# Optimization experiments

Hardware: AMD Instinct MI355X
Metric: run time of the kernel (lower is better)

The kernel has to match this reference:

```python
import jax, jax.numpy as jnp
import numpy as np

N_NODES = 100_000
N_EDGES = 1_600_000
D = 128
BN_EPS = 1e-5
GIN_EPS = 0.0  # GINConv default eps, train_eps=False


def setup_inputs() -> dict:
    key = jax.random.key(0)
    ks = jax.random.split(key, 8)
    x = jax.random.normal(ks[0], (N_NODES, D), dtype=jnp.float32)
    edge_index = jax.random.randint(ks[1], (2, N_EDGES), 0, N_NODES, dtype=jnp.int64)
    s = 1.0 / np.sqrt(D)
    W1 = jax.random.uniform(ks[2], (D, D), jnp.float32, -s, s)
    b1 = jax.random.uniform(ks[3], (D,), jnp.float32, -s, s)
    W2 = jax.random.uniform(ks[4], (D, D), jnp.float32, -s, s)
    b2 = jax.random.uniform(ks[5], (D,), jnp.float32, -s, s)
    W3 = jax.random.uniform(ks[6], (D, D), jnp.float32, -s, s)
    g1 = jnp.ones((D,), jnp.float32)
    be1 = jnp.zeros((D,), jnp.float32)
    g2 = jnp.ones((D,), jnp.float32)
    be2 = jnp.zeros((D,), jnp.float32)
    return {"x": x, "edge_index": edge_index,
            "W1": W1, "b1": b1, "g1": g1, "be1": be1,
            "W2": W2, "b2": b2, "g2": g2, "be2": be2,
            "W3": W3}


def _batchnorm(h, gamma, beta):
    # training-mode BatchNorm1d over node dim with biased variance
    mean = jnp.mean(h, axis=0)
    var = jnp.mean(jnp.square(h - mean), axis=0)
    return (h - mean) * jax.lax.rsqrt(var + BN_EPS) * gamma + beta


def reference(x, edge_index, W1, b1, g1, be1, W2, b2, g2, be2, W3):
    src, dst = edge_index[0], edge_index[1]
    # GIN aggregation: (1+eps)*x_i + sum_{j->i} x_j  (scatter-add over edges)
    agg = jax.ops.segment_sum(x[src], dst, num_segments=N_NODES)
    h = (1.0 + GIN_EPS) * x + agg
    # MLP: Linear+BN+ReLU x2, then Linear (no bias)
    h = jax.nn.relu(_batchnorm(h @ W1.T + b1, g1, be1))
    h = jax.nn.relu(_batchnorm(h @ W2.T + b2, g2, be2))
    h = h @ W3.T
    # GINLayer final activation (bn=None)
    return jax.nn.relu(h)
```

## Files before the change

### kernel.cpp

```cpp
#include <hip/hip_runtime.h>

#define NN 100000
#define NE 1600000
#define DD 128
#define NCB 196
#define TILE 2048
#define NTILE 782
#define SREP 32
#define WPAD 17408

typedef __attribute__((ext_vector_type(8))) short bf16x8;
typedef __attribute__((ext_vector_type(4))) float f32x4;

union u4bf8 { uint4 u; bf16x8 v; };

__device__ __forceinline__ ushort f2bf(float f) {
    union { float f; uint i; } v; v.f = f;
    uint i = v.i;
    return (ushort)((i + 0x7fffu + ((i >> 16) & 1u)) >> 16);
}
__device__ __forceinline__ float bf2f(ushort u) {
    union { uint i; float f; } v; v.i = ((uint)u) << 16; return v.f;
}
__device__ __forceinline__ float blo(uint v) { return bf2f((ushort)(v & 0xffffu)); }
__device__ __forceinline__ float bhi(uint v) { return bf2f((ushort)(v >> 16)); }

__global__ __launch_bounds__(256) void k_xbh(const float* __restrict__ x,
                                             uint* __restrict__ xb,
                                             const int* __restrict__ ei,
                                             int* __restrict__ ghistP,
                                             const float* __restrict__ W1,
                                             const float* __restrict__ W2,
                                             const float* __restrict__ W3,
                                             ushort* __restrict__ Wbp) {
    __shared__ int h[NCB];
    int t = threadIdx.x;
    if (t < NCB) h[t] = 0;
    __syncthreads();
    int base = blockIdx.x * TILE;
#pragma unroll
    for (int i = 0; i < 8; ++i) {
        int e = base + i * 256 + t;
        if (e < NE) atomicAdd(&h[ei[NE + e] >> 9], 1);
    }
    int gid = blockIdx.x * 256 + t;
#pragma unroll
    for (int i = 0; i < 8; ++i) {
        int item = i * (NTILE * 256) + gid;
        if (item < NN * 16) {
            int n = item >> 4, q = item & 15;
            const float* xp = x + (size_t)n * DD + q * 8;
            float4 a = *(const float4*)xp;
            float4 b = *(const float4*)(xp + 4);
            uint4 pk;
            pk.x = (uint)f2bf(a.x) | ((uint)f2bf(a.y) << 16);
            pk.y = (uint)f2bf(a.z) | ((uint)f2bf(a.w) << 16);
            pk.z = (uint)f2bf(b.x) | ((uint)f2bf(b.y) << 16);
            pk.w = (uint)f2bf(b.z) | ((uint)f2bf(b.w) << 16);
            *(uint4*)(xb + (size_t)n * 64 + q * 4) = pk;
        }
    }
    int c = gid;
    if (c < 6144) {
        int l = c >> 11;
        int cc = c & 2047;
        int r = cc >> 4, c8 = (cc & 15) * 8;
        const float* Wl = (l == 0) ? W1 : (l == 1) ? W2 : W3;
        const float* p = Wl + r * DD + c8;
        float4 a = *(const float4*)p;
        float4 b = *(const float4*)(p + 4);
        uint4 pk;
        pk.x = (uint)f2bf(a.x) | ((uint)f2bf(a.y) << 16);
        pk.y = (uint)f2bf(a.z) | ((uint)f2bf(a.w) << 16);
        pk.z = (uint)f2bf(b.x) | ((uint)f2bf(b.y) << 16);
        pk.w = (uint)f2bf(b.z) | ((uint)f2bf(b.w) << 16);
        *(uint4*)&Wbp[(size_t)l * WPAD + r * 136 + c8] = pk;
    }
    __syncthreads();
    if (t < NCB && h[t] > 0) atomicAdd(&ghistP[t * 16], h[t]);
}

__global__ void k_cscan(const int* __restrict__ ghistP, int* __restrict__ cb,
                        int* __restrict__ gcurP) {
    __shared__ int sh[256];
    int t = threadIdx.x;
    int my = (t < NCB) ? ghistP[t * 16] : 0;
    sh[t] = my;
    __syncthreads();
    for (int o = 1; o < 256; o <<= 1) {
        int u = (t >= o) ? sh[t - o] : 0;
        __syncthreads();
        sh[t] += u;
        __syncthreads();
    }
    if (t < NCB) { int ex = sh[t] - my; cb[t] = ex; gcurP[t * 16] = ex; }
    if (t == NCB - 1) cb[NCB] = sh[t];
}

__global__ __launch_bounds__(256) void k_cscatter(const int* __restrict__ ei,
                                                  int* __restrict__ gcurP,
                                                  uint* __restrict__ buck) {
    __shared__ int h[NCB];
    __shared__ int tb[NCB];
    int t = threadIdx.x;
    if (t < NCB) h[t] = 0;
    __syncthreads();
    int base = blockIdx.x * TILE;
    uint vv[8]; int bb[8], rr[8];
#pragma unroll
    for (int i = 0; i < 8; ++i) {
        int e = base + i * 256 + t;
        bb[i] = -1;
        if (e < NE) {
            int s = ei[e], d = ei[NE + e];
            int b = d >> 9;
            bb[i] = b;
            vv[i] = (uint)s | ((uint)(d & 511) << 17);
            rr[i] = atomicAdd(&h[b], 1);
        }
    }
    __syncthreads();
    if (t < NCB && h[t] > 0) tb[t] = atomicAdd(&gcurP[t * 16], h[t]);
    __syncthreads();
#pragma unroll
    for (int i = 0; i < 8; ++i) {
        if (bb[i] >= 0) buck[tb[bb[i]] + rr[i]] = vv[i];
    }
}

__global__ __launch_bounds__(256) void k_fsort(const uint* __restrict__ buck,
                                               const int* __restrict__ cb,
                                               int* __restrict__ csr,
                                               int* __restrict__ rowp) {
    __shared__ int cnt[512];
    __shared__ int sd[256];
    int c = blockIdx.x, t = threadIdx.x;
    cnt[t] = 0; cnt[t + 256] = 0;
    __syncthreads();
    int s0 = cb[c], s1 = cb[c + 1];
    for (int i = s0 + t; i < s1; i += 256)
        atomicAdd(&cnt[(buck[i] >> 17) & 511], 1);
    __syncthreads();
    int p = cnt[2 * t], q = cnt[2 * t + 1];
    sd[t] = p + q;
    __syncthreads();
    for (int o = 1; o < 256; o <<= 1) {
        int u = (t >= o) ? sd[t - o] : 0;
        __syncthreads();
        sd[t] += u;
        __syncthreads();
    }
    int base = sd[t] - (p + q);
    rowp[c * 512 + 2 * t]     = s0 + base;
    rowp[c * 512 + 2 * t + 1] = s0 + base + p;
    __syncthreads();
    cnt[2 * t] = base;
    cnt[2 * t + 1] = base + p;
    __syncthreads();
    for (int i = s0 + t; i < s1; i += 256) {
        uint v = buck[i];
        int ld = (int)((v >> 17) & 511u);
        int pos = atomicAdd(&cnt[ld], 1);
        csr[s0 + pos] = (int)(v & 0x1FFFFu);
    }
}

#define B8(ACC0, ACC1, SJ, J)                                               \
    {                                                                       \
        int s0 = __shfl(SJ, J),     s1 = __shfl(SJ, J + 1);                 \
        int s2 = __shfl(SJ, J + 2), s3 = __shfl(SJ, J + 3);                 \
        int s4 = __shfl(SJ, J + 4), s5 = __shfl(SJ, J + 5);                 \
        int s6 = __shfl(SJ, J + 6), s7 = __shfl(SJ, J + 7);                 \
        uint v0 = xb[(size_t)s0 * 64 + lane], v1 = xb[(size_t)s1 * 64 + lane]; \
        uint v2 = xb[(size_t)s2 * 64 + lane], v3 = xb[(size_t)s3 * 64 + lane]; \
        uint v4 = xb[(size_t)s4 * 64 + lane], v5 = xb[(size_t)s5 * 64 + lane]; \
        uint v6 = xb[(size_t)s6 * 64 + lane], v7 = xb[(size_t)s7 * 64 + lane]; \
        ACC0 += blo(v0) + blo(v1) + blo(v2) + blo(v3)                       \
              + blo(v4) + blo(v5) + blo(v6) + blo(v7);                      \
        ACC1 += bhi(v0) + bhi(v1) + bhi(v2) + bhi(v3)                       \
              + bhi(v4) + bhi(v5) + bhi(v6) + bhi(v7);                      \
    }

__global__ __launch_bounds__(256) void k_gather(const uint* __restrict__ xb,
                                                const int* __restrict__ rowp,
                                                const int* __restrict__ csr,
                                                ushort* __restrict__ agg) {
    const int HALF = NN / 2;
    int wave = threadIdx.x >> 6, lane = threadIdx.x & 63;
    int w = blockIdx.x * 4 + wave;
    if (w >= HALF) return;
    int nA = w, nB = w + HALF;
    uint sA = xb[(size_t)nA * 64 + lane];
    uint sB = xb[(size_t)nB * 64 + lane];
    float a0 = blo(sA), a1 = bhi(sA);
    float b0 = blo(sB), b1 = bhi(sB);
    int iA = rowp[nA], eA = rowp[nA + 1];
    int iB = rowp[nB], eB = rowp[nB + 1];

    while (iA < eA || iB < eB) {
        int mA = eA - iA; if (mA > 64) mA = 64; if (mA < 0) mA = 0;
        int mB = eB - iB; if (mB > 64) mB = 64; if (mB < 0) mB = 0;
        int sjA = (lane < mA) ? csr[iA + lane] : 0;
        int sjB = (lane < mB) ? csr[iB + lane] : 0;
        int j = 0, k = 0;
        while (j + 8 <= mA && k + 8 <= mB) {
            int t0 = __shfl(sjA, j),     t1 = __shfl(sjA, j + 1);
            int t2 = __shfl(sjA, j + 2), t3 = __shfl(sjA, j + 3);
            int t4 = __shfl(sjA, j + 4), t5 = __shfl(sjA, j + 5);
            int t6 = __shfl(sjA, j + 6), t7 = __shfl(sjA, j + 7);
            int u0 = __shfl(sjB, k),     u1 = __shfl(sjB, k + 1);
            int u2 = __shfl(sjB, k + 2), u3 = __shfl(sjB, k + 3);
            int u4 = __shfl(sjB, k + 4), u5 = __shfl(sjB, k + 5);
            int u6 = __shfl(sjB, k + 6), u7 = __shfl(sjB, k + 7);
            uint vA0 = xb[(size_t)t0 * 64 + lane], vA1 = xb[(size_t)t1 * 64 + lane];
            uint vA2 = xb[(size_t)t2 * 64 + lane], vA3 = xb[(size_t)t3 * 64 + lane];
            uint vA4 = xb[(size_t)t4 * 64 + lane], vA5 = xb[(size_t)t5 * 64 + lane];
            uint vA6 = xb[(size_t)t6 * 64 + lane], vA7 = xb[(size_t)t7 * 64 + lane];
            uint vB0 = xb[(size_t)u0 * 64 + lane], vB1 = xb[(size_t)u1 * 64 + lane];
            uint vB2 = xb[(size_t)u2 * 64 + lane], vB3 = xb[(size_t)u3 * 64 + lane];
            uint vB4 = xb[(size_t)u4 * 64 + lane], vB5 = xb[(size_t)u5 * 64 + lane];
            uint vB6 = xb[(size_t)u6 * 64 + lane], vB7 = xb[(size_t)u7 * 64 + lane];
            a0 += blo(vA0) + blo(vA1) + blo(vA2) + blo(vA3)
                + blo(vA4) + blo(vA5) + blo(vA6) + blo(vA7);
            a1 += bhi(vA0) + bhi(vA1) + bhi(vA2) + bhi(vA3)
                + bhi(vA4) + bhi(vA5) + bhi(vA6) + bhi(vA7);
            b0 += blo(vB0) + blo(vB1) + blo(vB2) + blo(vB3)
                + blo(vB4) + blo(vB5) + blo(vB6) + blo(vB7);
            b1 += bhi(vB0) + bhi(vB1) + bhi(vB2) + bhi(vB3)
                + bhi(vB4) + bhi(vB5) + bhi(vB6) + bhi(vB7);
            j += 8; k += 8;
        }
        while (j + 8 <= mA) { B8(a0, a1, sjA, j) j += 8; }
        while (k + 8 <= mB) { B8(b0, b1, sjB, k) k += 8; }
        while (j < mA && k < mB) {
            int t = __shfl(sjA, j); int u = __shfl(sjB, k);
            uint vA = xb[(size_t)t * 64 + lane];
            uint vB = xb[(size_t)u * 64 + lane];
            a0 += blo(vA); a1 += bhi(vA);
            b0 += blo(vB); b1 += bhi(vB);
            ++j; ++k;
        }
        while (j < mA) {
            int t = __shfl(sjA, j++);
            uint vA = xb[(size_t)t * 64 + lane];
            a0 += blo(vA); a1 += bhi(vA);
        }
        while (k < mB) {
            int u = __shfl(sjB, k++);
            uint vB = xb[(size_t)u * 64 + lane];
            b0 += blo(vB); b1 += bhi(vB);
        }
        iA += mA; iB += mB;
    }

    uint pkA = (uint)f2bf(a0) | ((uint)f2bf(a1) << 16);
    uint pkB = (uint)f2bf(b0) | ((uint)f2bf(b1) << 16);
    ((uint*)(agg + (size_t)nA * DD))[lane] = pkA;
    ((uint*)(agg + (size_t)nB * DD))[lane] = pkB;
}

template <int MODE>
__global__ __launch_bounds__(256) void k_gemm(const ushort* __restrict__ Ain,
                                              const ushort* __restrict__ Wp,
                                              const float* __restrict__ bias,
                                              const float* __restrict__ statsIn,
                                              const float* __restrict__ g,
                                              const float* __restrict__ be,
                                              void* __restrict__ Outv,
                                              float* __restrict__ statsOut) {
    __shared__ __align__(16) char smem[DD * 136 * 2];
    ushort* lw = (ushort*)smem;
    float* sm32 = (float*)smem;
    __shared__ float red[2][4][DD];
    __shared__ float lac[2 * DD];

    int tid = threadIdx.x;
#pragma unroll
    for (int it = 0; it < 8; ++it) {
        int o8 = (it * 256 + tid) * 8;
        *(uint4*)&lw[o8] = *(const uint4*)&Wp[o8];
    }
    if (tid < 128) {
        int o8 = 16384 + tid * 8;
        *(uint4*)&lw[o8] = *(const uint4*)&Wp[o8];
    }
    if constexpr (MODE != 1) {
        if (tid < DD) {
            float S = 0.f, Q = 0.f;
#pragma unroll
            for (int r = 0; r < SREP; ++r) {
                S += statsIn[(r << 8) + tid];
                Q += statsIn[(r << 8) + DD + tid];
            }
            float inv = 1.f / (float)NN;
            float mean = S * inv;
            float var = Q * inv - mean * mean;
            float a = g[tid] * rsqrtf(var + 1e-5f);
            lac[tid] = a;
            lac[DD + tid] = be[tid] - mean * a;
        }
    }
    __syncthreads();

    int wave = tid >> 6, lane = tid & 63;
    int lm = lane & 15, quad = lane >> 4;
    int row0 = blockIdx.x * 64 + wave * 16;
    int arow = row0 + lm;
    int ar = (arow < NN) ? arow : 0;

    bf16x8 afrag[4];
#pragma unroll
    for (int kb = 0; kb < 4; ++kb) {
        int k0 = kb * 32 + quad * 8;
        const ushort* ap = Ain + (size_t)ar * DD + k0;
        u4bf8 u; u.u = *(const uint4*)ap;
        if constexpr (MODE == 1) {
            afrag[kb] = u.v;
        } else {
            uint pk[4] = {u.u.x, u.u.y, u.u.z, u.u.w};
            bf16x8 af;
#pragma unroll
            for (int jj = 0; jj < 4; ++jj) {
                int k = k0 + jj * 2;
                float v0 = blo(pk[jj]);
                float v1 = bhi(pk[jj]);
                v0 = fmaxf(fmaf(v0, lac[k], lac[DD + k]), 0.f);
                v1 = fmaxf(fmaf(v1, lac[k + 1], lac[DD + k + 1]), 0.f);
                af[jj * 2]     = (short)f2bf(v0);
                af[jj * 2 + 1] = (short)f2bf(v1);
            }
            afrag[kb] = af;
        }
    }

    f32x4 acc[8];
#pragma unroll
    for (int nt = 0; nt < 8; ++nt) {
        float bv = (MODE == 3) ? 0.f : bias[nt * 16 + lm];
        acc[nt] = (f32x4){bv, bv, bv, bv};
    }

#pragma unroll
    for (int kb = 0; kb < 4; ++kb) {
#pragma unroll
        for (int nt = 0; nt < 8; ++nt) {
            bf16x8 bfrag = *(const bf16x8*)&lw[(nt * 16 + lm) * 136 + kb * 32 + quad * 8];
            acc[nt] = __builtin_amdgcn_mfma_f32_16x16x32_bf16(afrag[kb], bfrag, acc[nt], 0, 0, 0);
        }
    }

    float csum[8], csq[8];
    if constexpr (MODE != 3) {
#pragma unroll
        for (int nt = 0; nt < 8; ++nt) {
            float s = 0.f, q = 0.f;
#pragma unroll
            for (int r = 0; r < 4; ++r) {
                int row = row0 + quad * 4 + r;
                float v = acc[nt][r];
                if (row < NN) { s += v; q += v * v; }
            }
            csum[nt] = s; csq[nt] = q;
        }
    }

    __syncthreads();
#pragma unroll
    for (int nt = 0; nt < 8; ++nt) {
#pragma unroll
        for (int r = 0; r < 4; ++r) {
            int lrow = wave * 16 + quad * 4 + r;
            float v = acc[nt][r];
            if (MODE == 3) v = fmaxf(v, 0.f);
            sm32[lrow * 132 + nt * 16 + lm] = v;
        }
    }
    __syncthreads();

    {
        int row = tid >> 2, seg = tid & 3;
        int grow = blockIdx.x * 64 + row;
        if (grow < NN) {
            const float* rp = sm32 + row * 132 + seg * 32;
            if constexpr (MODE == 3) {
                float* Out32 = (float*)Outv;
#pragma unroll
                for (int u = 0; u < 8; ++u) {
                    float4 o;
                    o.x = rp[u * 4]; o.y = rp[u * 4 + 1];
                    o.z = rp[u * 4 + 2]; o.w = rp[u * 4 + 3];
                    *(float4*)&Out32[(size_t)grow * DD + seg * 32 + u * 4] = o;
                }
            } else {
                ushort* Out16 = (ushort*)Outv;
#pragma unroll
                for (int u = 0; u < 4; ++u) {
                    uint4 pk;
                    pk.x = (uint)f2bf(rp[u * 8])     | ((uint)f2bf(rp[u * 8 + 1]) << 16);
                    pk.y = (uint)f2bf(rp[u * 8 + 2]) | ((uint)f2bf(rp[u * 8 + 3]) << 16);
                    pk.z = (uint)f2bf(rp[u * 8 + 4]) | ((uint)f2bf(rp[u * 8 + 5]) << 16);
                    pk.w = (uint)f2bf(rp[u * 8 + 6]) | ((uint)f2bf(rp[u * 8 + 7]) << 16);
                    *(uint4*)&Out16[(size_t)grow * DD + seg * 32 + u * 8] = pk;
                }
            }
        }
    }

    if constexpr (MODE != 3) {
#pragma unroll
        for (int nt = 0; nt < 8; ++nt) {
            float s = csum[nt], q = csq[nt];
            s += __shfl_down(s, 16, 64); q += __shfl_down(q, 16, 64);
            s += __shfl_down(s, 32, 64); q += __shfl_down(q, 32, 64);
            if (quad == 0) {
                red[0][wave][nt * 16 + lm] = s;
                red[1][wave][nt * 16 + lm] = q;
            }
        }
        __syncthreads();
        if (tid < DD) {
            float S = red[0][0][tid] + red[0][1][tid] + red[0][2][tid] + red[0][3][tid];
            float Q = red[1][0][tid] + red[1][1][tid] + red[1][2][tid] + red[1][3][tid];
            int rep = (blockIdx.x & (SREP - 1)) << 8;
            atomicAdd(&statsOut[rep + tid], S);
            atomicAdd(&statsOut[rep + DD + tid], Q);
        }
    }
}

extern "C" void kernel_launch(void* const* d_in, const int* in_sizes, int n_in,
                              void* d_out, int out_size, void* d_ws, size_t ws_size,
                              hipStream_t stream) {
    const float* x   = (const float*)d_in[0];
    const int* ei    = (const int*)d_in[1];
    const float* W1  = (const float*)d_in[2];
    const float* b1  = (const float*)d_in[3];
    const float* g1  = (const float*)d_in[4];
    const float* be1 = (const float*)d_in[5];
    const float* W2  = (const float*)d_in[6];
    const float* b2  = (const float*)d_in[7];
    const float* g2  = (const float*)d_in[8];
    const float* be2 = (const float*)d_in[9];
    const float* W3  = (const float*)d_in[10];

    float* stats  = (float*)d_ws;
    float* stats2 = stats + SREP * 256;
    int* ghistP   = (int*)(stats2 + SREP * 256);
    ushort* Wbp   = (ushort*)(ghistP + NCB * 16);
    int* cb       = (int*)(Wbp + 3 * WPAD);
    int* gcurP    = cb + NCB + 4;
    int* rowp     = gcurP + NCB * 16;
    uint* buck    = (uint*)(rowp + NCB * 512 + 4);
    int* csr      = (int*)(buck + NE);
    ushort* agg   = (ushort*)(((uintptr_t)(csr + NE) + 15) & ~(uintptr_t)15);
    uint* xb     = (uint*)d_out;
    ushort* t1   = (ushort*)d_out + (size_t)NN * DD;
    ushort* t2   = agg;
    float* outp  = (float*)d_out;

    int gblk = (NN + 63) / 64;
    hipMemsetAsync(stats, 0, (2 * SREP * 256) * sizeof(float) + NCB * 16 * sizeof(int), stream);
    k_xbh<<<NTILE, 256, 0, stream>>>(x, xb, ei, ghistP, W1, W2, W3, Wbp);
    k_cscan<<<1, 256, 0, stream>>>(ghistP, cb, gcurP);
    k_cscatter<<<NTILE, 256, 0, stream>>>(ei, gcurP, buck);
    k_fsort<<<NCB, 256, 0, stream>>>(buck, cb, csr, rowp);
    k_gather<<<(NN / 2 + 3) / 4, 256, 0, stream>>>(xb, rowp, csr, agg);
    k_gemm<1><<<gblk, 256, 0, stream>>>(agg, Wbp, b1, nullptr, nullptr, nullptr, t1, stats);
    k_gemm<2><<<gblk, 256, 0, stream>>>(t1, Wbp + WPAD, b2, stats, g1, be1, t2, stats2);
    k_gemm<3><<<gblk, 256, 0, stream>>>(t2, Wbp + 2 * WPAD, nullptr, stats2, g2, be2, outp, nullptr);
}
```

Measured before the change: 313.7 us.

## Process four row sub-tiles per GEMM block and store results directly

Each GEMM block now handles 256 rows in four 64-row sub-tiles, so the 128x128 weight tile is loaded into LDS once per 256 rows instead of once per 64 rows, and there are a quarter as many blocks. The LDS staging of the output tile and its coalesced vector stores are removed; each lane writes scalar bf16 or fp32 values straight to global memory. This cuts weight reloads and block-level syncs, but the direct stores are narrow and strided (2-byte writes across 16 columns), which may coalesce poorly. Fewer blocks also reduces parallelism.

```diff
diff --git a/kernel.cpp b/kernel.cpp
--- a/kernel.cpp
+++ b/kernel.cpp
@@ -8,6 +8,7 @@
 #define NTILE 782
 #define SREP 32
 #define WPAD 17408
+#define GROWS 256
 
 typedef __attribute__((ext_vector_type(8))) short bf16x8;
 typedef __attribute__((ext_vector_type(4))) float f32x4;
@@ -268,9 +269,7 @@
                                               const float* __restrict__ be,
                                               void* __restrict__ Outv,
                                               float* __restrict__ statsOut) {
-    __shared__ __align__(16) char smem[DD * 136 * 2];
-    ushort* lw = (ushort*)smem;
-    float* sm32 = (float*)smem;
+    __shared__ __align__(16) ushort lw[DD * 136];
     __shared__ float red[2][4][DD];
     __shared__ float lac[2 * DD];
 
@@ -304,103 +303,73 @@
 
     int wave = tid >> 6, lane = tid & 63;
     int lm = lane & 15, quad = lane >> 4;
-    int row0 = blockIdx.x * 64 + wave * 16;
-    int arow = row0 + lm;
-    int ar = (arow < NN) ? arow : 0;
-
-    bf16x8 afrag[4];
-#pragma unroll
-    for (int kb = 0; kb < 4; ++kb) {
-        int k0 = kb * 32 + quad * 8;
-        const ushort* ap = Ain + (size_t)ar * DD + k0;
-        u4bf8 u; u.u = *(const uint4*)ap;
-        if constexpr (MODE == 1) {
-            afrag[kb] = u.v;
-        } else {
-            uint pk[4] = {u.u.x, u.u.y, u.u.z, u.u.w};
-            bf16x8 af;
-#pragma unroll
-            for (int jj = 0; jj < 4; ++jj) {
-                int k = k0 + jj * 2;
-                float v0 = blo(pk[jj]);
-                float v1 = bhi(pk[jj]);
-                v0 = fmaxf(fmaf(v0, lac[k], lac[DD + k]), 0.f);
-                v1 = fmaxf(fmaf(v1, lac[k + 1], lac[DD + k + 1]), 0.f);
-                af[jj * 2]     = (short)f2bf(v0);
-                af[jj * 2 + 1] = (short)f2bf(v1);
+    ushort* Out16 = (ushort*)Outv;
+    float* Out32 = (float*)Outv;
+
+    float csum[8], csq[8];
+#pragma unroll
+    for (int nt = 0; nt < 8; ++nt) { csum[nt] = 0.f; csq[nt] = 0.f; }
+
+#pragma unroll
+    for (int sub = 0; sub < 4; ++sub) {
+        int row0 = blockIdx.x * GROWS + sub * 64 + wave * 16;
+        int arow = row0 + lm;
+        int ar = (arow < NN) ? arow : 0;
+
+        bf16x8 afrag[4];
+#pragma unroll
+        for (int kb = 0; kb < 4; ++kb) {
+            int k0 = kb * 32 + quad * 8;
+            const ushort* ap = Ain + (size_t)ar * DD + k0;
+            u4bf8 u; u.u = *(const uint4*)ap;
+            if constexpr (MODE == 1) {
+                afrag[kb] = u.v;
+            } else {
+                uint pk[4] = {u.u.x, u.u.y, u.u.z, u.u.w};
+                bf16x8 af;
+#pragma unroll
+                for (int jj = 0; jj < 4; ++jj) {
+                    int k = k0 + jj * 2;
+                    float v0 = blo(pk[jj]);
+                    float v1 = bhi(pk[jj]);
+                    v0 = fmaxf(fmaf(v0, lac[k], lac[DD + k]), 0.f);
+                    v1 = fmaxf(fmaf(v1, lac[k + 1], lac[DD + k + 1]), 0.f);
+                    af[jj * 2]     = (short)f2bf(v0);
+                    af[jj * 2 + 1] = (short)f2bf(v1);
+                }
+                afrag[kb] = af;
             }
-            afrag[kb] = af;
-        }
-    }
-
-    f32x4 acc[8];
-#pragma unroll
-    for (int nt = 0; nt < 8; ++nt) {
-        float bv = (MODE == 3) ? 0.f : bias[nt * 16 + lm];
-        acc[nt] = (f32x4){bv, bv, bv, bv};
-    }
-
-#pragma unroll
-    for (int kb = 0; kb < 4; ++kb) {
+        }
+
+        f32x4 acc[8];
 #pragma unroll
         for (int nt = 0; nt < 8; ++nt) {
-            bf16x8 bfrag = *(const bf16x8*)&lw[(nt * 16 + lm) * 136 + kb * 32 + quad * 8];
-            acc[nt] = __builtin_amdgcn_mfma_f32_16x16x32_bf16(afrag[kb], bfrag, acc[nt], 0, 0, 0);
-        }
-    }
-
-    float csum[8], csq[8];
-    if constexpr (MODE != 3) {
+            float bv = (MODE == 3) ? 0.f : bias[nt * 16 + lm];
+            acc[nt] = (f32x4){bv, bv, bv, bv};
+        }
+
+#pragma unroll
+        for (int kb = 0; kb < 4; ++kb) {
+#pragma unroll
+            for (int nt = 0; nt < 8; ++nt) {
+                bf16x8 bfrag = *(const bf16x8*)&lw[(nt * 16 + lm) * 136 + kb * 32 + quad * 8];
+                acc[nt] = __builtin_amdgcn_mfma_f32_16x16x32_bf16(afrag[kb], bfrag, acc[nt], 0, 0, 0);
+            }
+        }
+
 #pragma unroll
         for (int nt = 0; nt < 8; ++nt) {
-            float s = 0.f, q = 0.f;
+            int col = nt * 16 + lm;
 #pragma unroll
             for (int r = 0; r < 4; ++r) {
                 int row = row0 + quad * 4 + r;
                 float v = acc[nt][r];
-                if (row < NN) { s += v; q += v * v; }
-            }
-            csum[nt] = s; csq[nt] = q;
-        }
-    }
-
-    __syncthreads();
-#pragma unroll
-    for (int nt = 0; nt < 8; ++nt) {
-#pragma unroll
-        for (int r = 0; r < 4; ++r) {
-            int lrow = wave * 16 + quad * 4 + r;
-            float v = acc[nt][r];
-            if (MODE == 3) v = fmaxf(v, 0.f);
-            sm32[lrow * 132 + nt * 16 + lm] = v;
-        }
-    }
-    __syncthreads();
-
-    {
-        int row = tid >> 2, seg = tid & 3;
-        int grow = blockIdx.x * 64 + row;
-        if (grow < NN) {
-            const float* rp = sm32 + row * 132 + seg * 32;
-            if constexpr (MODE == 3) {
-                float* Out32 = (float*)Outv;
-#pragma unroll
-                for (int u = 0; u < 8; ++u) {
-                    float4 o;
-                    o.x = rp[u * 4]; o.y = rp[u * 4 + 1];
-                    o.z = rp[u * 4 + 2]; o.w = rp[u * 4 + 3];
-                    *(float4*)&Out32[(size_t)grow * DD + seg * 32 + u * 4] = o;
-                }
-            } else {
-                ushort* Out16 = (ushort*)Outv;
-#pragma unroll
-                for (int u = 0; u < 4; ++u) {
-                    uint4 pk;
-                    pk.x = (uint)f2bf(rp[u * 8])     | ((uint)f2bf(rp[u * 8 + 1]) << 16);
-                    pk.y = (uint)f2bf(rp[u * 8 + 2]) | ((uint)f2bf(rp[u * 8 + 3]) << 16);
-                    pk.z = (uint)f2bf(rp[u * 8 + 4]) | ((uint)f2bf(rp[u * 8 + 5]) << 16);
-                    pk.w = (uint)f2bf(rp[u * 8 + 6]) | ((uint)f2bf(rp[u * 8 + 7]) << 16);
-                    *(uint4*)&Out16[(size_t)grow * DD + seg * 32 + u * 8] = pk;
+                if (MODE == 3) v = fmaxf(v, 0.f);
+                if (row < NN) {
+                    if constexpr (MODE == 3) Out32[(size_t)row * DD + col] = v;
+                    else Out16[(size_t)row * DD + col] = f2bf(v);
+                    csum[nt] += v;
+                    csq[nt] += v * v;
                 }
             }
         }
@@ -458,7 +427,7 @@
     ushort* t2   = agg;
     float* outp  = (float*)d_out;
 
-    int gblk = (NN + 63) / 64;
+    int gblk = (NN + GROWS - 1) / GROWS;
     hipMemsetAsync(stats, 0, (2 * SREP * 256) * sizeof(float) + NCB * 16 * sizeof(int), stream);
     k_xbh<<<NTILE, 256, 0, stream>>>(x, xb, ei, ghistP, W1, W2, W3, Wbp);
     k_cscan<<<1, 256, 0, stream>>>(ghistP, cb, gcurP);
```

New measurement: 303.3 us. 1.03x faster.
